# Kernel tuning notes

Measured on AMD Instinct MI355X. Metric: run time of the kernel, lower is better.

## Reference

```python
import jax, jax.numpy as jnp
import numpy as np

B, T = 1024, 512
X_DIM, H_DIM, Z_DIM = 24, 64, 16


def setup_inputs() -> dict:
    key = jax.random.key(0)
    ks = jax.random.split(key, 32)
    w = lambda k, s: jax.random.normal(k, s, jnp.float32) * 0.1
    H, X, Z = H_DIM, X_DIM, Z_DIM
    return {
        "src": jax.random.normal(ks[0], (B, T, X), jnp.float32),
        "eps": jax.random.normal(ks[1], (B, T, Z), jnp.float32),  # reparam noise
        # phi_x: Linear(X,H)+ReLU+Linear(H,H)+ReLU
        "Wx1": w(ks[2], (X, H)), "bx1": w(ks[3], (H,)),
        "Wx2": w(ks[4], (H, H)), "bx2": w(ks[5], (H,)),
        # phi_z: Linear(Z,H)+ReLU
        "Wz": w(ks[6], (Z, H)), "bz": w(ks[7], (H,)),
        # enc: Linear(2H,H)+ReLU+Linear(H,H)+ReLU
        "We1": w(ks[8], (2 * H, H)), "be1": w(ks[9], (H,)),
        "We2": w(ks[10], (H, H)), "be2": w(ks[11], (H,)),
        "Wem": w(ks[12], (H, Z)), "bem": w(ks[13], (Z,)),
        "Wes": w(ks[14], (H, Z)), "bes": w(ks[15], (Z,)),
        # GRU(2H -> H), bias=False; PyTorch gate order r,z,n
        "Wih": w(ks[16], (2 * H, 3 * H)), "Whh": w(ks[17], (H, 3 * H)),
        "Wf1": w(ks[18], (H, H)), "bf1": w(ks[19], (H,)),
        "Wf2": w(ks[20], (H, H // 2)), "bf2": w(ks[21], (H // 2,)),
        "Wf3": w(ks[22], (H // 2, 1)), "bf3": w(ks[23], (1,)),
    }


def _forward(src, eps, Wx1, bx1, Wx2, bx2, Wz, bz, We1, be1, We2, be2,
             Wem, bem, Wes, bes, Wih, Whh, Wf1, bf1, Wf2, bf2, Wf3, bf3):
    relu, sp, sig = jax.nn.relu, jax.nn.softplus, jax.nn.sigmoid
    Bsz = src.shape[0]
    H = Whh.shape[0]

    def step(carry, inp):
        h, _ = carry                      # h: [B, H] (n_layers=1 GRU)
        x_t, e_t = inp                    # [B, X], [B, Z]
        phi_x = relu(relu(x_t @ Wx1 + bx1) @ Wx2 + bx2)
        enc_t = relu(relu(jnp.concatenate([phi_x, h], 1) @ We1 + be1) @ We2 + be2)
        enc_mean = enc_t @ Wem + bem
        enc_std = sp(enc_t @ Wes + bes)
        z_t = e_t * enc_std + enc_mean    # reparameterized sample
        phi_z = relu(z_t @ Wz + bz)
        # GRU cell (bias=False), PyTorch gate order r, z, n
        gi = jnp.concatenate([phi_x, phi_z], 1) @ Wih   # [B, 3H]
        gh = h @ Whh                                    # [B, 3H]
        gir, giz, gin = jnp.split(gi, 3, axis=1)
        ghr, ghz, ghn = jnp.split(gh, 3, axis=1)
        r = sig(gir + ghr)
        u = sig(giz + ghz)
        n = jnp.tanh(gin + r * ghn)
        h_new = (1.0 - u) * n + u * h
        return (h_new, phi_z), None

    h0 = jnp.zeros((Bsz, H), src.dtype)
    xs = jnp.swapaxes(src, 0, 1)   # [T, B, X]
    es = jnp.swapaxes(eps, 0, 1)   # [T, B, Z]
    (_, phi_z), _ = jax.lax.scan(step, (h0, h0), (xs, es))
    out = relu(phi_z @ Wf1 + bf1)
    out = relu(out @ Wf2 + bf2)
    pred = out @ Wf3 + bf3
    return (pred, phi_z)


def reference(src, eps, Wx1, bx1, Wx2, bx2, Wz, bz, We1, be1, We2, be2,
              Wem, bem, Wes, bes, Wih, Whh, Wf1, bf1, Wf2, bf2, Wf3, bf3):
    return _forward(src, eps, Wx1, bx1, Wx2, bx2, Wz, bz, We1, be1, We2, be2,
                    Wem, bem, Wes, bes, Wih, Whh, Wf1, bf1, Wf2, bf2, Wf3, bf3)
```

## Files before the change

kernel.cpp:

```cpp
#include <hip/hip_runtime.h>

#define TT 512
#define BB 1024
#define XD 24
#define ZD 16

typedef __attribute__((ext_vector_type(2))) _Float16 h2t;
typedef __attribute__((ext_vector_type(4))) _Float16 half4;
typedef __attribute__((ext_vector_type(4))) float f32x4;
typedef unsigned long long u64;

__device__ __forceinline__ f32x4 MFMA16(half4 a, half4 b, f32x4 c) {
#if defined(__HIP_DEVICE_COMPILE__)
    return __builtin_amdgcn_mfma_f32_16x16x16f16(a, b, c, 0, 0, 0);
#else
    return c;
#endif
}

__device__ __forceinline__ float rcpf(float x) {
#if defined(__HIP_DEVICE_COMPILE__)
    return __builtin_amdgcn_rcpf(x);
#else
    return 1.0f / x;
#endif
}

__device__ __forceinline__ h2t pkrtz(float a, float b) {
#if defined(__HIP_DEVICE_COMPILE__)
    union { __attribute__((ext_vector_type(2))) __fp16 f; h2t h; } c;
    c.f = __builtin_amdgcn_cvt_pkrtz(a, b);
    return c.h;
#else
    h2t r; r[0] = (_Float16)a; r[1] = (_Float16)b; return r;
#endif
}

#define BAR() asm volatile("s_waitcnt lgkmcnt(0)\n\ts_barrier" ::: "memory")

__device__ __forceinline__ f32x4 Z4() { return (f32x4){0.f, 0.f, 0.f, 0.f}; }

__device__ __forceinline__ float sigm(float x) { return rcpf(1.0f + __expf(-x)); }

__device__ __forceinline__ float tanh_fast(float x) {
    return 1.0f - 2.0f * rcpf(1.0f + __expf(2.0f * x));
}

__device__ __forceinline__ float softplus_f(float x) {
    return fmaxf(x, 0.0f) + __logf(1.0f + __expf(-fabsf(x)));
}

__device__ __forceinline__ half4 ldw(const float* W, int N, int Kreal, int Nreal,
                                     int k0, int o0, int lane) {
    int col = o0 + (lane & 15);
    int kb = k0 + ((lane >> 4) << 2);
    half4 r;
#pragma unroll
    for (int j = 0; j < 4; ++j) {
        int k = kb + j;
        float v = (k < Kreal && col < Nreal) ? W[(size_t)k * N + col] : 0.0f;
        r[j] = (_Float16)v;
    }
    return r;
}

__device__ __forceinline__ half4 cvt_relu(f32x4 a) {
    union { h2t p[2]; half4 h; } c;
    c.p[0] = pkrtz(fmaxf(a[0], 0.f), fmaxf(a[1], 0.f));
    c.p[1] = pkrtz(fmaxf(a[2], 0.f), fmaxf(a[3], 0.f));
    return c.h;
}

__device__ __forceinline__ half4 cvt4(f32x4 a) {
    union { h2t p[2]; half4 h; } c;
    c.p[0] = pkrtz(a[0], a[1]);
    c.p[1] = pkrtz(a[2], a[3]);
    return c.h;
}

__device__ __forceinline__ half4 cvt4_rne(f32x4 a) {
    half4 r;
#pragma unroll
    for (int q = 0; q < 4; ++q) r[q] = (_Float16)a[q];
    return r;
}

__device__ __forceinline__ f32x4 ldb4(const float* b, int o, int lgr) {
    return *reinterpret_cast<const f32x4*>(b + o * 16 + lgr * 4);
}

__device__ __forceinline__ u64 h2u(half4 h) {
    union { half4 h; u64 u; } c; c.h = h; return c.u;
}
__device__ __forceinline__ half4 u2h(u64 u) {
    union { half4 h; u64 u; } c; c.u = u; return c.h;
}

__global__ __launch_bounds__(256, 1) void vrnn_kernel(
    const float* __restrict__ src, const float* __restrict__ eps,
    const float* __restrict__ Wx1, const float* __restrict__ bx1,
    const float* __restrict__ Wx2, const float* __restrict__ bx2,
    const float* __restrict__ Wz,  const float* __restrict__ bz,
    const float* __restrict__ We1, const float* __restrict__ be1,
    const float* __restrict__ We2, const float* __restrict__ be2,
    const float* __restrict__ Wem, const float* __restrict__ bem,
    const float* __restrict__ Wes, const float* __restrict__ bes,
    const float* __restrict__ Wih, const float* __restrict__ Whh,
    const float* __restrict__ Wf1, const float* __restrict__ bf1,
    const float* __restrict__ Wf2, const float* __restrict__ bf2,
    const float* __restrict__ Wf3, const float* __restrict__ bf3,
    float* __restrict__ out)
{
    __shared__ u64 AXB[4 * 64];
    __shared__ u64 A1B[4 * 64];
    __shared__ u64 HB[4 * 64];
    __shared__ u64 PXB[2][4 * 64];

    const int tid = threadIdx.x;
    const int ws = tid >> 6;
    const int lane = tid & 63;
    const int lcol = lane & 15;
    const int lgr = lane >> 4;
    const int r0 = blockIdx.x * 16;
    const int o0w = ws * 16;

    half4 wx1f[2], wx2f[4], we1f[8], we2f[4][4], wemf[4], wesf[4], wzf4[4];
    wx1f[0] = ldw(Wx1, 64, 24, 64, 0, o0w, lane);
    wx1f[1] = ldw(Wx1, 64, 24, 64, 16, o0w, lane);
#pragma unroll
    for (int kt = 0; kt < 4; ++kt) wx2f[kt] = ldw(Wx2, 64, 64, 64, kt * 16, o0w, lane);
#pragma unroll
    for (int kt = 0; kt < 8; ++kt) we1f[kt] = ldw(We1, 64, 128, 64, kt * 16, o0w, lane);
#pragma unroll
    for (int o = 0; o < 4; ++o)
#pragma unroll
        for (int kt = 0; kt < 4; ++kt) we2f[o][kt] = ldw(We2, 64, 64, 64, kt * 16, o * 16, lane);
#pragma unroll
    for (int kt = 0; kt < 4; ++kt) {
        wemf[kt] = ldw(Wem, 16, 64, 16, kt * 16, 0, lane);
        wesf[kt] = ldw(Wes, 16, 64, 16, kt * 16, 0, lane);
    }
#pragma unroll
    for (int o = 0; o < 4; ++o) wzf4[o] = ldw(Wz, 64, 16, 64, 0, o * 16, lane);
    half4 wihf[3][8], whhf[3][4];
#pragma unroll
    for (int g = 0; g < 3; ++g) {
#pragma unroll
        for (int kt = 0; kt < 8; ++kt) wihf[g][kt] = ldw(Wih, 192, 128, 192, kt * 16, g * 64 + o0w, lane);
#pragma unroll
        for (int kt = 0; kt < 4; ++kt) whhf[g][kt] = ldw(Whh, 192, 64, 192, kt * 16, g * 64 + o0w, lane);
    }
    const f32x4 B1 = ldb4(bx1, ws, lgr), B2 = ldb4(bx2, ws, lgr);
    const f32x4 BE1 = ldb4(be1, ws, lgr);
    f32x4 BE2[4], BZf[4];
#pragma unroll
    for (int o = 0; o < 4; ++o) {
        BE2[o] = ldb4(be2, o, lgr);
        BZf[o] = ldb4(bz, o, lgr);
    }
    const f32x4 BM = ldb4(bem, 0, lgr), BS = ldb4(bes, 0, lgr);

    const float* xb_ = src + (size_t)(r0 + lcol) * TT * XD;
    const float* eb_ = eps + (size_t)(r0 + lcol) * TT * ZD;
    float* po = out + BB + (size_t)(r0 + lcol) * 64;

    f32x4 fx0 = *reinterpret_cast<const f32x4*>(xb_ + lgr * 4);
    f32x4 fx1 = Z4();
    if (lgr < 2) fx1 = *reinterpret_cast<const f32x4*>(xb_ + 16 + lgr * 4);
    {
        half4 x0 = cvt4(fx0), x1 = cvt4(fx1);
        f32x4 a = MFMA16(wx1f[1], x1, MFMA16(wx1f[0], x0, B1));
        AXB[ws * 64 + lane] = h2u(cvt_relu(a));
    }
    HB[ws * 64 + lane] = 0ull;
    f32x4 hD = Z4();
    BAR();
    {
        half4 axb[4];
#pragma unroll
        for (int kt = 0; kt < 4; ++kt) axb[kt] = u2h(AXB[kt * 64 + lane]);
        f32x4 a = B2;
#pragma unroll
        for (int kt = 0; kt < 4; ++kt) a = MFMA16(wx2f[kt], axb[kt], a);
        PXB[0][ws * 64 + lane] = h2u(cvt_relu(a));
    }
    fx0 = *reinterpret_cast<const f32x4*>(xb_ + XD + lgr * 4);
    fx1 = Z4();
    if (lgr < 2) fx1 = *reinterpret_cast<const f32x4*>(xb_ + XD + 16 + lgr * 4);
    f32x4 fe = *reinterpret_cast<const f32x4*>(eb_ + lgr * 4);
    BAR();

    half4 pxb[4], pzb[4];

#pragma unroll 1
    for (int t = 0; t < TT; ++t) {
        const size_t t1 = (size_t)((t + 1) & (TT - 1));
        const size_t t2 = (size_t)((t + 2) & (TT - 1));

        half4 hb[4];
#pragma unroll
        for (int kt = 0; kt < 4; ++kt) hb[kt] = u2h(HB[kt * 64 + lane]);
#pragma unroll
        for (int kt = 0; kt < 4; ++kt) pxb[kt] = u2h(PXB[t & 1][kt * 64 + lane]);

        {
            f32x4 a = BE1;
#pragma unroll
            for (int kt = 0; kt < 4; ++kt) a = MFMA16(we1f[kt], pxb[kt], a);
            f32x4 b = Z4();
#pragma unroll
            for (int kt = 0; kt < 4; ++kt) b = MFMA16(we1f[4 + kt], hb[kt], b);
            A1B[ws * 64 + lane] = h2u(cvt_relu(a + b));
        }
        f32x4 ga[3];
#pragma unroll
        for (int g = 0; g < 3; ++g) {
            f32x4 a = MFMA16(whhf[g][1], hb[1], MFMA16(whhf[g][0], hb[0], Z4()));
            f32x4 b = MFMA16(whhf[g][3], hb[3], MFMA16(whhf[g][2], hb[2], Z4()));
            ga[g] = a + b;
        }
        {
            half4 x0 = cvt4(fx0), x1 = cvt4(fx1);
            f32x4 s = MFMA16(wx1f[1], x1, MFMA16(wx1f[0], x0, B1));
            AXB[ws * 64 + lane] = h2u(cvt_relu(s));
            fx0 = *reinterpret_cast<const f32x4*>(xb_ + t2 * XD + lgr * 4);
            fx1 = Z4();
            if (lgr < 2) fx1 = *reinterpret_cast<const f32x4*>(xb_ + t2 * XD + 16 + lgr * 4);
        }
        BAR();

        half4 a1b[4];
#pragma unroll
        for (int kt = 0; kt < 4; ++kt) a1b[kt] = u2h(A1B[kt * 64 + lane]);
        half4 enb[4];
#pragma unroll
        for (int o = 0; o < 4; ++o) {
            f32x4 a = MFMA16(we2f[o][1], a1b[1], MFMA16(we2f[o][0], a1b[0], BE2[o]));
            f32x4 b = MFMA16(we2f[o][3], a1b[3], MFMA16(we2f[o][2], a1b[2], Z4()));
            enb[o] = cvt_relu(a + b);
        }
        f32x4 am = MFMA16(wemf[1], enb[1], MFMA16(wemf[0], enb[0], BM));
        f32x4 am2 = MFMA16(wemf[3], enb[3], MFMA16(wemf[2], enb[2], Z4()));
        f32x4 as_ = MFMA16(wesf[1], enb[1], MFMA16(wesf[0], enb[0], BS));
        f32x4 as2 = MFMA16(wesf[3], enb[3], MFMA16(wesf[2], enb[2], Z4()));
        f32x4 eC = fe;
        fe = *reinterpret_cast<const f32x4*>(eb_ + t1 * ZD + lgr * 4);
        f32x4 zD;
#pragma unroll
        for (int q = 0; q < 4; ++q)
            zD[q] = eC[q] * softplus_f(as_[q] + as2[q]) + (am[q] + am2[q]);
        half4 zb = cvt4(zD);
#pragma unroll
        for (int o = 0; o < 4; ++o) {
            f32x4 a = MFMA16(wzf4[o], zb, BZf[o]);
            if (t == TT - 1 && ws == 0) {
                f32x4 pr;
#pragma unroll
                for (int q = 0; q < 4; ++q) pr[q] = fmaxf(a[q], 0.0f);
                *reinterpret_cast<f32x4*>(po + o * 16 + lgr * 4) = pr;
            }
            pzb[o] = cvt_relu(a);
        }
        f32x4 gi[3];
#pragma unroll
        for (int g = 0; g < 3; ++g) {
            f32x4 p = (g < 2) ? ga[g] : Z4();
#pragma unroll
            for (int kt = 0; kt < 4; ++kt) p = MFMA16(wihf[g][kt], pxb[kt], p);
            f32x4 q = Z4();
#pragma unroll
            for (int kt = 0; kt < 4; ++kt) q = MFMA16(wihf[g][4 + kt], pzb[kt], q);
            gi[g] = p + q;
        }
#pragma unroll
        for (int q = 0; q < 4; ++q) {
            float rr = sigm(gi[0][q]);
            float uu = sigm(gi[1][q]);
            float nn = tanh_fast(gi[2][q] + rr * ga[2][q]);
            hD[q] = (1.0f - uu) * nn + uu * hD[q];
        }
        HB[ws * 64 + lane] = h2u(cvt4_rne(hD));
        {
            half4 axb[4];
#pragma unroll
            for (int kt = 0; kt < 4; ++kt) axb[kt] = u2h(AXB[kt * 64 + lane]);
            f32x4 s = B2;
#pragma unroll
            for (int kt = 0; kt < 4; ++kt) s = MFMA16(wx2f[kt], axb[kt], s);
            PXB[(t + 1) & 1][ws * 64 + lane] = h2u(cvt_relu(s));
        }
        BAR();
    }

    if (ws == 0) {
        half4 wf1t[4][4], wf2t[2][4], wf3t[2];
#pragma unroll
        for (int o = 0; o < 4; ++o)
#pragma unroll
            for (int kt = 0; kt < 4; ++kt) wf1t[o][kt] = ldw(Wf1, 64, 64, 64, kt * 16, o * 16, lane);
#pragma unroll
        for (int o = 0; o < 2; ++o)
#pragma unroll
            for (int kt = 0; kt < 4; ++kt) wf2t[o][kt] = ldw(Wf2, 32, 64, 32, kt * 16, o * 16, lane);
        wf3t[0] = ldw(Wf3, 1, 32, 1, 0, 0, lane);
        wf3t[1] = ldw(Wf3, 1, 32, 1, 16, 0, lane);

        half4 o1b[4];
#pragma unroll
        for (int o = 0; o < 4; ++o) {
            f32x4 a = ldb4(bf1, o, lgr);
#pragma unroll
            for (int kt = 0; kt < 4; ++kt) a = MFMA16(wf1t[o][kt], pzb[kt], a);
            o1b[o] = cvt_relu(a);
        }
        half4 o2b[2];
#pragma unroll
        for (int o = 0; o < 2; ++o) {
            f32x4 a = ldb4(bf2, o, lgr);
#pragma unroll
            for (int kt = 0; kt < 4; ++kt) a = MFMA16(wf2t[o][kt], o1b[kt], a);
            o2b[o] = cvt_relu(a);
        }
        float b3 = bf3[0];
        f32x4 p = (f32x4){b3, b3, b3, b3};
        p = MFMA16(wf3t[0], o2b[0], p);
        p = MFMA16(wf3t[1], o2b[1], p);
        if (lgr == 0) out[r0 + lcol] = p[0];
    }
}

extern "C" void kernel_launch(void* const* d_in, const int* in_sizes, int n_in,
                              void* d_out, int out_size, void* d_ws, size_t ws_size,
                              hipStream_t stream) {
    (void)in_sizes; (void)n_in; (void)d_ws; (void)ws_size; (void)out_size;
    const float* src = (const float*)d_in[0];
    const float* eps = (const float*)d_in[1];
    const float* Wx1 = (const float*)d_in[2];
    const float* bx1 = (const float*)d_in[3];
    const float* Wx2 = (const float*)d_in[4];
    const float* bx2 = (const float*)d_in[5];
    const float* Wz  = (const float*)d_in[6];
    const float* bz  = (const float*)d_in[7];
    const float* We1 = (const float*)d_in[8];
    const float* be1 = (const float*)d_in[9];
    const float* We2 = (const float*)d_in[10];
    const float* be2 = (const float*)d_in[11];
    const float* Wem = (const float*)d_in[12];
    const float* bem = (const float*)d_in[13];
    const float* Wes = (const float*)d_in[14];
    const float* bes = (const float*)d_in[15];
    const float* Wih = (const float*)d_in[16];
    const float* Whh = (const float*)d_in[17];
    const float* Wf1 = (const float*)d_in[18];
    const float* bf1 = (const float*)d_in[19];
    const float* Wf2 = (const float*)d_in[20];
    const float* bf2 = (const float*)d_in[21];
    const float* Wf3 = (const float*)d_in[22];
    const float* bf3 = (const float*)d_in[23];
    float* out = (float*)d_out;

    hipLaunchKernelGGL(vrnn_kernel, dim3(BB / 16), dim3(256), 0, stream,
                       src, eps, Wx1, bx1, Wx2, bx2, Wz, bz, We1, be1, We2, be2,
                       Wem, bem, Wes, bes, Wih, Whh, Wf1, bf1, Wf2, bf2, Wf3, bf3, out);
}
```

Measured before the change: 912.8 us.

## Replicate enc layer-1 per wave and double-buffer buffers to drop a barrier

Each wave now computes the full 64-wide first encoder layer (all four output tiles) in registers instead of one tile shared through LDS. This removes the A1B buffer and the mid-step barrier, leaving one barrier per timestep. The HB and AXB buffers are double-buffered, and the phi_x second layer is software-pipelined one extra step ahead. The cost is four times the We1 MFMA work per wave and more weight registers (32 extra half4), which adds register pressure.

```diff
diff --git a/kernel.cpp b/kernel.cpp
--- a/kernel.cpp
+++ b/kernel.cpp
@@ -111,9 +111,8 @@
     const float* __restrict__ Wf3, const float* __restrict__ bf3,
     float* __restrict__ out)
 {
-    __shared__ u64 AXB[4 * 64];
-    __shared__ u64 A1B[4 * 64];
-    __shared__ u64 HB[4 * 64];
+    __shared__ u64 AXB[2][4 * 64];
+    __shared__ u64 HB[2][4 * 64];
     __shared__ u64 PXB[2][4 * 64];
 
     const int tid = threadIdx.x;
@@ -124,13 +123,15 @@
     const int r0 = blockIdx.x * 16;
     const int o0w = ws * 16;
 
-    half4 wx1f[2], wx2f[4], we1f[8], we2f[4][4], wemf[4], wesf[4], wzf4[4];
+    half4 wx1f[2], wx2f[4], we1f[4][8], we2f[4][4], wemf[4], wesf[4], wzf4[4];
     wx1f[0] = ldw(Wx1, 64, 24, 64, 0, o0w, lane);
     wx1f[1] = ldw(Wx1, 64, 24, 64, 16, o0w, lane);
 #pragma unroll
     for (int kt = 0; kt < 4; ++kt) wx2f[kt] = ldw(Wx2, 64, 64, 64, kt * 16, o0w, lane);
 #pragma unroll
-    for (int kt = 0; kt < 8; ++kt) we1f[kt] = ldw(We1, 64, 128, 64, kt * 16, o0w, lane);
+    for (int o = 0; o < 4; ++o)
+#pragma unroll
+        for (int kt = 0; kt < 8; ++kt) we1f[o][kt] = ldw(We1, 64, 128, 64, kt * 16, o * 16, lane);
 #pragma unroll
     for (int o = 0; o < 4; ++o)
 #pragma unroll
@@ -151,11 +152,11 @@
         for (int kt = 0; kt < 4; ++kt) whhf[g][kt] = ldw(Whh, 192, 64, 192, kt * 16, g * 64 + o0w, lane);
     }
     const f32x4 B1 = ldb4(bx1, ws, lgr), B2 = ldb4(bx2, ws, lgr);
-    const f32x4 BE1 = ldb4(be1, ws, lgr);
-    f32x4 BE2[4], BZf[4];
+    f32x4 BE1f[4], BE2f[4], BZf[4];
 #pragma unroll
     for (int o = 0; o < 4; ++o) {
-        BE2[o] = ldb4(be2, o, lgr);
+        BE1f[o] = ldb4(be1, o, lgr);
+        BE2f[o] = ldb4(be2, o, lgr);
         BZf[o] = ldb4(bz, o, lgr);
     }
     const f32x4 BM = ldb4(bem, 0, lgr), BS = ldb4(bes, 0, lgr);
@@ -170,23 +171,31 @@
     {
         half4 x0 = cvt4(fx0), x1 = cvt4(fx1);
         f32x4 a = MFMA16(wx1f[1], x1, MFMA16(wx1f[0], x0, B1));
-        AXB[ws * 64 + lane] = h2u(cvt_relu(a));
-    }
-    HB[ws * 64 + lane] = 0ull;
+        AXB[1][ws * 64 + lane] = h2u(cvt_relu(a));
+    }
+    HB[0][ws * 64 + lane] = 0ull;
     f32x4 hD = Z4();
+    fx0 = *reinterpret_cast<const f32x4*>(xb_ + XD + lgr * 4);
+    fx1 = Z4();
+    if (lgr < 2) fx1 = *reinterpret_cast<const f32x4*>(xb_ + XD + 16 + lgr * 4);
     BAR();
     {
         half4 axb[4];
 #pragma unroll
-        for (int kt = 0; kt < 4; ++kt) axb[kt] = u2h(AXB[kt * 64 + lane]);
+        for (int kt = 0; kt < 4; ++kt) axb[kt] = u2h(AXB[1][kt * 64 + lane]);
         f32x4 a = B2;
 #pragma unroll
         for (int kt = 0; kt < 4; ++kt) a = MFMA16(wx2f[kt], axb[kt], a);
         PXB[0][ws * 64 + lane] = h2u(cvt_relu(a));
     }
-    fx0 = *reinterpret_cast<const f32x4*>(xb_ + XD + lgr * 4);
+    {
+        half4 x0 = cvt4(fx0), x1 = cvt4(fx1);
+        f32x4 a = MFMA16(wx1f[1], x1, MFMA16(wx1f[0], x0, B1));
+        AXB[0][ws * 64 + lane] = h2u(cvt_relu(a));
+    }
+    fx0 = *reinterpret_cast<const f32x4*>(xb_ + 2 * XD + lgr * 4);
     fx1 = Z4();
-    if (lgr < 2) fx1 = *reinterpret_cast<const f32x4*>(xb_ + XD + 16 + lgr * 4);
+    if (lgr < 2) fx1 = *reinterpret_cast<const f32x4*>(xb_ + 2 * XD + 16 + lgr * 4);
     f32x4 fe = *reinterpret_cast<const f32x4*>(eb_ + lgr * 4);
     BAR();
 
@@ -194,24 +203,18 @@
 
 #pragma unroll 1
     for (int t = 0; t < TT; ++t) {
+        const int cur = t & 1, nxt = (t + 1) & 1;
         const size_t t1 = (size_t)((t + 1) & (TT - 1));
-        const size_t t2 = (size_t)((t + 2) & (TT - 1));
-
-        half4 hb[4];
-#pragma unroll
-        for (int kt = 0; kt < 4; ++kt) hb[kt] = u2h(HB[kt * 64 + lane]);
-#pragma unroll
-        for (int kt = 0; kt < 4; ++kt) pxb[kt] = u2h(PXB[t & 1][kt * 64 + lane]);
-
-        {
-            f32x4 a = BE1;
-#pragma unroll
-            for (int kt = 0; kt < 4; ++kt) a = MFMA16(we1f[kt], pxb[kt], a);
-            f32x4 b = Z4();
-#pragma unroll
-            for (int kt = 0; kt < 4; ++kt) b = MFMA16(we1f[4 + kt], hb[kt], b);
-            A1B[ws * 64 + lane] = h2u(cvt_relu(a + b));
-        }
+        const size_t t3 = (size_t)((t + 3) & (TT - 1));
+
+        half4 hb[4], axb[4];
+#pragma unroll
+        for (int kt = 0; kt < 4; ++kt) hb[kt] = u2h(HB[cur][kt * 64 + lane]);
+#pragma unroll
+        for (int kt = 0; kt < 4; ++kt) pxb[kt] = u2h(PXB[cur][kt * 64 + lane]);
+#pragma unroll
+        for (int kt = 0; kt < 4; ++kt) axb[kt] = u2h(AXB[cur][kt * 64 + lane]);
+
         f32x4 ga[3];
 #pragma unroll
         for (int g = 0; g < 3; ++g) {
@@ -219,23 +222,37 @@
             f32x4 b = MFMA16(whhf[g][3], hb[3], MFMA16(whhf[g][2], hb[2], Z4()));
             ga[g] = a + b;
         }
+
+        half4 a1b[4];
+#pragma unroll
+        for (int o = 0; o < 4; ++o) {
+            f32x4 a = MFMA16(we1f[o][1], pxb[1], MFMA16(we1f[o][0], pxb[0], BE1f[o]));
+            f32x4 b = MFMA16(we1f[o][3], pxb[3], MFMA16(we1f[o][2], pxb[2], Z4()));
+            f32x4 c = MFMA16(we1f[o][5], hb[1], MFMA16(we1f[o][4], hb[0], Z4()));
+            f32x4 d = MFMA16(we1f[o][7], hb[3], MFMA16(we1f[o][6], hb[2], Z4()));
+            a1b[o] = cvt_relu((a + b) + (c + d));
+        }
+
         {
             half4 x0 = cvt4(fx0), x1 = cvt4(fx1);
             f32x4 s = MFMA16(wx1f[1], x1, MFMA16(wx1f[0], x0, B1));
-            AXB[ws * 64 + lane] = h2u(cvt_relu(s));
-            fx0 = *reinterpret_cast<const f32x4*>(xb_ + t2 * XD + lgr * 4);
+            AXB[nxt][ws * 64 + lane] = h2u(cvt_relu(s));
+            fx0 = *reinterpret_cast<const f32x4*>(xb_ + t3 * XD + lgr * 4);
             fx1 = Z4();
-            if (lgr < 2) fx1 = *reinterpret_cast<const f32x4*>(xb_ + t2 * XD + 16 + lgr * 4);
-        }
-        BAR();
-
-        half4 a1b[4];
-#pragma unroll
-        for (int kt = 0; kt < 4; ++kt) a1b[kt] = u2h(A1B[kt * 64 + lane]);
+            if (lgr < 2) fx1 = *reinterpret_cast<const f32x4*>(xb_ + t3 * XD + 16 + lgr * 4);
+        }
+
+        {
+            f32x4 s = B2;
+#pragma unroll
+            for (int kt = 0; kt < 4; ++kt) s = MFMA16(wx2f[kt], axb[kt], s);
+            PXB[nxt][ws * 64 + lane] = h2u(cvt_relu(s));
+        }
+
         half4 enb[4];
 #pragma unroll
         for (int o = 0; o < 4; ++o) {
-            f32x4 a = MFMA16(we2f[o][1], a1b[1], MFMA16(we2f[o][0], a1b[0], BE2[o]));
+            f32x4 a = MFMA16(we2f[o][1], a1b[1], MFMA16(we2f[o][0], a1b[0], BE2f[o]));
             f32x4 b = MFMA16(we2f[o][3], a1b[3], MFMA16(we2f[o][2], a1b[2], Z4()));
             enb[o] = cvt_relu(a + b);
         }
@@ -250,6 +267,7 @@
         for (int q = 0; q < 4; ++q)
             zD[q] = eC[q] * softplus_f(as_[q] + as2[q]) + (am[q] + am2[q]);
         half4 zb = cvt4(zD);
+
 #pragma unroll
         for (int o = 0; o < 4; ++o) {
             f32x4 a = MFMA16(wzf4[o], zb, BZf[o]);
@@ -261,6 +279,7 @@
             }
             pzb[o] = cvt_relu(a);
         }
+
         f32x4 gi[3];
 #pragma unroll
         for (int g = 0; g < 3; ++g) {
@@ -279,16 +298,8 @@
             float nn = tanh_fast(gi[2][q] + rr * ga[2][q]);
             hD[q] = (1.0f - uu) * nn + uu * hD[q];
         }
-        HB[ws * 64 + lane] = h2u(cvt4_rne(hD));
-        {
-            half4 axb[4];
-#pragma unroll
-            for (int kt = 0; kt < 4; ++kt) axb[kt] = u2h(AXB[kt * 64 + lane]);
-            f32x4 s = B2;
-#pragma unroll
-            for (int kt = 0; kt < 4; ++kt) s = MFMA16(wx2f[kt], axb[kt], s);
-            PXB[(t + 1) & 1][ws * 64 + lane] = h2u(cvt_relu(s));
-        }
+        HB[nxt][ws * 64 + lane] = h2u(cvt4_rne(hD));
+
         BAR();
     }
 
```

Result: slower. 1.023 ms (+12.1%).

## Switch recurrent matmuls to 16x16x32 f16 MFMA with paired LDS layout

Applied to the files above, without the earlier changes.

Replaces most 16x16x16 MFMA chains (phi_x, encoder, GRU hidden and input-from-phi_x gates) with the double-K 16x16x32 instruction, halving the MFMA issue count on the serial per-step path. The LDS activation buffers are re-laid out so two adjacent 16-wide K tiles are stored interleaved, letting each lane fetch an 8-half fragment with one 128-bit load. The AXB buffer load is moved earlier, right after the first barrier, and the GRU update is rewritten to use one fewer multiply. The new layout adds indexing complexity and relies on the gfx950 instruction being available.

```diff
diff --git a/kernel.cpp b/kernel.cpp
--- a/kernel.cpp
+++ b/kernel.cpp
@@ -7,12 +7,20 @@
 
 typedef __attribute__((ext_vector_type(2))) _Float16 h2t;
 typedef __attribute__((ext_vector_type(4))) _Float16 half4;
+typedef __attribute__((ext_vector_type(8))) _Float16 half8;
 typedef __attribute__((ext_vector_type(4))) float f32x4;
 typedef unsigned long long u64;
 
 __device__ __forceinline__ f32x4 MFMA16(half4 a, half4 b, f32x4 c) {
 #if defined(__HIP_DEVICE_COMPILE__)
     return __builtin_amdgcn_mfma_f32_16x16x16f16(a, b, c, 0, 0, 0);
+#else
+    return c;
+#endif
+}
+__device__ __forceinline__ f32x4 MFMA32(half8 a, half8 b, f32x4 c) {
+#if defined(__HIP_DEVICE_COMPILE__)
+    return __builtin_amdgcn_mfma_f32_16x16x32_f16(a, b, c, 0, 0, 0);
 #else
     return c;
 #endif
@@ -63,6 +71,19 @@
     }
     return r;
 }
+__device__ __forceinline__ half8 ldw32(const float* W, int N, int Kreal, int Nreal,
+                                       int k0, int o0, int lane) {
+    int col = o0 + (lane & 15);
+    int kb = k0 + ((lane >> 4) << 3);
+    half8 r;
+#pragma unroll
+    for (int j = 0; j < 8; ++j) {
+        int k = kb + j;
+        float v = (k < Kreal && col < Nreal) ? W[(size_t)k * N + col] : 0.0f;
+        r[j] = (_Float16)v;
+    }
+    return r;
+}
 
 __device__ __forceinline__ half4 cvt_relu(f32x4 a) {
     union { h2t p[2]; half4 h; } c;
@@ -70,20 +91,24 @@
     c.p[1] = pkrtz(fmaxf(a[2], 0.f), fmaxf(a[3], 0.f));
     return c.h;
 }
-
 __device__ __forceinline__ half4 cvt4(f32x4 a) {
     union { h2t p[2]; half4 h; } c;
     c.p[0] = pkrtz(a[0], a[1]);
     c.p[1] = pkrtz(a[2], a[3]);
     return c.h;
 }
-
 __device__ __forceinline__ half4 cvt4_rne(f32x4 a) {
     half4 r;
 #pragma unroll
     for (int q = 0; q < 4; ++q) r[q] = (_Float16)a[q];
     return r;
 }
+__device__ __forceinline__ half8 xfrag(f32x4 A, f32x4 B) {
+    union { h2t p[4]; half8 h; } c;
+    c.p[0] = pkrtz(A[0], A[1]); c.p[1] = pkrtz(A[2], A[3]);
+    c.p[2] = pkrtz(B[0], B[1]); c.p[3] = pkrtz(B[2], B[3]);
+    return c.h;
+}
 
 __device__ __forceinline__ f32x4 ldb4(const float* b, int o, int lgr) {
     return *reinterpret_cast<const f32x4*>(b + o * 16 + lgr * 4);
@@ -92,8 +117,12 @@
 __device__ __forceinline__ u64 h2u(half4 h) {
     union { half4 h; u64 u; } c; c.h = h; return c.u;
 }
-__device__ __forceinline__ half4 u2h(u64 u) {
-    union { half4 h; u64 u; } c; c.u = u; return c.h;
+
+__device__ __forceinline__ void st_pair(u64* B, int w, int c, u64 v) {
+    *reinterpret_cast<u64*>(reinterpret_cast<char*>(B) + ((w >> 1) * 256 + c * 16 + (w & 1) * 8)) = v;
+}
+__device__ __forceinline__ half8 ld_pair(const u64* B, int pair, int c) {
+    return *reinterpret_cast<const half8*>(reinterpret_cast<const char*>(B) + pair * 256 + c * 16);
 }
 
 __global__ __launch_bounds__(256, 1) void vrnn_kernel(
@@ -111,10 +140,10 @@
     const float* __restrict__ Wf3, const float* __restrict__ bf3,
     float* __restrict__ out)
 {
-    __shared__ u64 AXB[4 * 64];
-    __shared__ u64 A1B[4 * 64];
-    __shared__ u64 HB[4 * 64];
-    __shared__ u64 PXB[2][4 * 64];
+    __shared__ alignas(16) u64 AXB[256];
+    __shared__ alignas(16) u64 A1B[256];
+    __shared__ alignas(16) u64 HB[256];
+    __shared__ alignas(16) u64 PXB[2][256];
 
     const int tid = threadIdx.x;
     const int ws = tid >> 6;
@@ -123,18 +152,19 @@
     const int lgr = lane >> 4;
     const int r0 = blockIdx.x * 16;
     const int o0w = ws * 16;
-
-    half4 wx1f[2], wx2f[4], we1f[8], we2f[4][4], wemf[4], wesf[4], wzf4[4];
-    wx1f[0] = ldw(Wx1, 64, 24, 64, 0, o0w, lane);
-    wx1f[1] = ldw(Wx1, 64, 24, 64, 16, o0w, lane);
-#pragma unroll
-    for (int kt = 0; kt < 4; ++kt) wx2f[kt] = ldw(Wx2, 64, 64, 64, kt * 16, o0w, lane);
-#pragma unroll
-    for (int kt = 0; kt < 8; ++kt) we1f[kt] = ldw(We1, 64, 128, 64, kt * 16, o0w, lane);
+    const int wsl = ws * 4 + lgr;
+
+    half8 wx1w = ldw32(Wx1, 64, 24, 64, 0, o0w, lane);
+    half8 wx2w[2], we1w[4], we2w[4][2];
+#pragma unroll
+    for (int kt = 0; kt < 2; ++kt) wx2w[kt] = ldw32(Wx2, 64, 64, 64, kt * 32, o0w, lane);
+#pragma unroll
+    for (int kt = 0; kt < 4; ++kt) we1w[kt] = ldw32(We1, 64, 128, 64, kt * 32, o0w, lane);
 #pragma unroll
     for (int o = 0; o < 4; ++o)
 #pragma unroll
-        for (int kt = 0; kt < 4; ++kt) we2f[o][kt] = ldw(We2, 64, 64, 64, kt * 16, o * 16, lane);
+        for (int kt = 0; kt < 2; ++kt) we2w[o][kt] = ldw32(We2, 64, 64, 64, kt * 32, o * 16, lane);
+    half4 wemf[4], wesf[4], wzf4[4];
 #pragma unroll
     for (int kt = 0; kt < 4; ++kt) {
         wemf[kt] = ldw(Wem, 16, 64, 16, kt * 16, 0, lane);
@@ -142,20 +172,25 @@
     }
 #pragma unroll
     for (int o = 0; o < 4; ++o) wzf4[o] = ldw(Wz, 64, 16, 64, 0, o * 16, lane);
-    half4 wihf[3][8], whhf[3][4];
+    half8 wihw[3][2], whhw[3][2];
+    half4 wihz[3][4];
 #pragma unroll
     for (int g = 0; g < 3; ++g) {
 #pragma unroll
-        for (int kt = 0; kt < 8; ++kt) wihf[g][kt] = ldw(Wih, 192, 128, 192, kt * 16, g * 64 + o0w, lane);
-#pragma unroll
-        for (int kt = 0; kt < 4; ++kt) whhf[g][kt] = ldw(Whh, 192, 64, 192, kt * 16, g * 64 + o0w, lane);
+        for (int kt = 0; kt < 2; ++kt) {
+            wihw[g][kt] = ldw32(Wih, 192, 128, 192, kt * 32, g * 64 + o0w, lane);
+            whhw[g][kt] = ldw32(Whh, 192, 64, 192, kt * 32, g * 64 + o0w, lane);
+        }
+#pragma unroll
+        for (int kt = 0; kt < 4; ++kt)
+            wihz[g][kt] = ldw(Wih, 192, 128, 192, 64 + kt * 16, g * 64 + o0w, lane);
     }
     const f32x4 B1 = ldb4(bx1, ws, lgr), B2 = ldb4(bx2, ws, lgr);
     const f32x4 BE1 = ldb4(be1, ws, lgr);
-    f32x4 BE2[4], BZf[4];
+    f32x4 BE2f[4], BZf[4];
 #pragma unroll
     for (int o = 0; o < 4; ++o) {
-        BE2[o] = ldb4(be2, o, lgr);
+        BE2f[o] = ldb4(be2, o, lgr);
         BZf[o] = ldb4(bz, o, lgr);
     }
     const f32x4 BM = ldb4(bem, 0, lgr), BS = ldb4(bes, 0, lgr);
@@ -164,81 +199,76 @@
     const float* eb_ = eps + (size_t)(r0 + lcol) * TT * ZD;
     float* po = out + BB + (size_t)(r0 + lcol) * 64;
 
-    f32x4 fx0 = *reinterpret_cast<const f32x4*>(xb_ + lgr * 4);
-    f32x4 fx1 = Z4();
-    if (lgr < 2) fx1 = *reinterpret_cast<const f32x4*>(xb_ + 16 + lgr * 4);
+    f32x4 fxA = Z4(), fxB = Z4();
+    if (lgr < 3) {
+        fxA = *reinterpret_cast<const f32x4*>(xb_ + lgr * 8);
+        fxB = *reinterpret_cast<const f32x4*>(xb_ + lgr * 8 + 4);
+    }
     {
-        half4 x0 = cvt4(fx0), x1 = cvt4(fx1);
-        f32x4 a = MFMA16(wx1f[1], x1, MFMA16(wx1f[0], x0, B1));
-        AXB[ws * 64 + lane] = h2u(cvt_relu(a));
-    }
-    HB[ws * 64 + lane] = 0ull;
+        f32x4 s = MFMA32(wx1w, xfrag(fxA, fxB), B1);
+        st_pair(A1B, wsl, lcol, h2u(cvt_relu(s)));
+    }
+    HB[tid] = 0ull;
     f32x4 hD = Z4();
+    fxA = Z4(); fxB = Z4();
+    if (lgr < 3) {
+        fxA = *reinterpret_cast<const f32x4*>(xb_ + XD + lgr * 8);
+        fxB = *reinterpret_cast<const f32x4*>(xb_ + XD + lgr * 8 + 4);
+    }
     BAR();
     {
-        half4 axb[4];
-#pragma unroll
-        for (int kt = 0; kt < 4; ++kt) axb[kt] = u2h(AXB[kt * 64 + lane]);
-        f32x4 a = B2;
-#pragma unroll
-        for (int kt = 0; kt < 4; ++kt) a = MFMA16(wx2f[kt], axb[kt], a);
-        PXB[0][ws * 64 + lane] = h2u(cvt_relu(a));
-    }
-    fx0 = *reinterpret_cast<const f32x4*>(xb_ + XD + lgr * 4);
-    fx1 = Z4();
-    if (lgr < 2) fx1 = *reinterpret_cast<const f32x4*>(xb_ + XD + 16 + lgr * 4);
+        half8 a1p0 = ld_pair(A1B, lgr, lcol);
+        half8 a1p1 = ld_pair(A1B, 4 + lgr, lcol);
+        f32x4 s = MFMA32(wx2w[1], a1p1, MFMA32(wx2w[0], a1p0, B2));
+        st_pair(PXB[0], wsl, lcol, h2u(cvt_relu(s)));
+    }
     f32x4 fe = *reinterpret_cast<const f32x4*>(eb_ + lgr * 4);
     BAR();
 
-    half4 pxb[4], pzb[4];
+    half4 pzb[4];
+    half8 pxp0, pxp1;
 
 #pragma unroll 1
     for (int t = 0; t < TT; ++t) {
+        const int cur = t & 1, nxt = cur ^ 1;
         const size_t t1 = (size_t)((t + 1) & (TT - 1));
         const size_t t2 = (size_t)((t + 2) & (TT - 1));
 
-        half4 hb[4];
-#pragma unroll
-        for (int kt = 0; kt < 4; ++kt) hb[kt] = u2h(HB[kt * 64 + lane]);
-#pragma unroll
-        for (int kt = 0; kt < 4; ++kt) pxb[kt] = u2h(PXB[t & 1][kt * 64 + lane]);
+        half8 hp0 = ld_pair(HB, lgr, lcol);
+        half8 hp1 = ld_pair(HB, 4 + lgr, lcol);
+        pxp0 = ld_pair(PXB[cur], lgr, lcol);
+        pxp1 = ld_pair(PXB[cur], 4 + lgr, lcol);
 
         {
-            f32x4 a = BE1;
-#pragma unroll
-            for (int kt = 0; kt < 4; ++kt) a = MFMA16(we1f[kt], pxb[kt], a);
-            f32x4 b = Z4();
-#pragma unroll
-            for (int kt = 0; kt < 4; ++kt) b = MFMA16(we1f[4 + kt], hb[kt], b);
-            A1B[ws * 64 + lane] = h2u(cvt_relu(a + b));
+            f32x4 a = MFMA32(we1w[1], pxp1, MFMA32(we1w[0], pxp0, BE1));
+            f32x4 b = MFMA32(we1w[3], hp1, MFMA32(we1w[2], hp0, Z4()));
+            st_pair(A1B, wsl, lcol, h2u(cvt_relu(a + b)));
         }
         f32x4 ga[3];
 #pragma unroll
-        for (int g = 0; g < 3; ++g) {
-            f32x4 a = MFMA16(whhf[g][1], hb[1], MFMA16(whhf[g][0], hb[0], Z4()));
-            f32x4 b = MFMA16(whhf[g][3], hb[3], MFMA16(whhf[g][2], hb[2], Z4()));
-            ga[g] = a + b;
-        }
+        for (int g = 0; g < 3; ++g)
+            ga[g] = MFMA32(whhw[g][1], hp1, MFMA32(whhw[g][0], hp0, Z4()));
         {
-            half4 x0 = cvt4(fx0), x1 = cvt4(fx1);
-            f32x4 s = MFMA16(wx1f[1], x1, MFMA16(wx1f[0], x0, B1));
-            AXB[ws * 64 + lane] = h2u(cvt_relu(s));
-            fx0 = *reinterpret_cast<const f32x4*>(xb_ + t2 * XD + lgr * 4);
-            fx1 = Z4();
-            if (lgr < 2) fx1 = *reinterpret_cast<const f32x4*>(xb_ + t2 * XD + 16 + lgr * 4);
+            f32x4 s = MFMA32(wx1w, xfrag(fxA, fxB), B1);
+            st_pair(AXB, wsl, lcol, h2u(cvt_relu(s)));
+            fxA = Z4(); fxB = Z4();
+            if (lgr < 3) {
+                fxA = *reinterpret_cast<const f32x4*>(xb_ + t2 * XD + lgr * 8);
+                fxB = *reinterpret_cast<const f32x4*>(xb_ + t2 * XD + lgr * 8 + 4);
+            }
         }
         BAR();
 
-        half4 a1b[4];
-#pragma unroll
-        for (int kt = 0; kt < 4; ++kt) a1b[kt] = u2h(A1B[kt * 64 + lane]);
+        half8 a1p0 = ld_pair(A1B, lgr, lcol);
+        half8 a1p1 = ld_pair(A1B, 4 + lgr, lcol);
+        half8 axp0 = ld_pair(AXB, lgr, lcol);
+        half8 axp1 = ld_pair(AXB, 4 + lgr, lcol);
+
         half4 enb[4];
 #pragma unroll
-        for (int o = 0; o < 4; ++o) {
-            f32x4 a = MFMA16(we2f[o][1], a1b[1], MFMA16(we2f[o][0], a1b[0], BE2[o]));
-            f32x4 b = MFMA16(we2f[o][3], a1b[3], MFMA16(we2f[o][2], a1b[2], Z4()));
-            enb[o] = cvt_relu(a + b);
-        }
+        for (int o = 0; o < 4; ++o)
+            enb[o] = cvt_relu(MFMA32(we2w[o][1], a1p1, MFMA32(we2w[o][0], a1p0, BE2f[o])));
+
         f32x4 am = MFMA16(wemf[1], enb[1], MFMA16(wemf[0], enb[0], BM));
         f32x4 am2 = MFMA16(wemf[3], enb[3], MFMA16(wemf[2], enb[2], Z4()));
         f32x4 as_ = MFMA16(wesf[1], enb[1], MFMA16(wesf[0], enb[0], BS));
@@ -250,6 +280,7 @@
         for (int q = 0; q < 4; ++q)
             zD[q] = eC[q] * softplus_f(as_[q] + as2[q]) + (am[q] + am2[q]);
         half4 zb = cvt4(zD);
+
 #pragma unroll
         for (int o = 0; o < 4; ++o) {
             f32x4 a = MFMA16(wzf4[o], zb, BZf[o]);
@@ -261,33 +292,27 @@
             }
             pzb[o] = cvt_relu(a);
         }
+
         f32x4 gi[3];
 #pragma unroll
         for (int g = 0; g < 3; ++g) {
-            f32x4 p = (g < 2) ? ga[g] : Z4();
-#pragma unroll
-            for (int kt = 0; kt < 4; ++kt) p = MFMA16(wihf[g][kt], pxb[kt], p);
-            f32x4 q = Z4();
-#pragma unroll
-            for (int kt = 0; kt < 4; ++kt) q = MFMA16(wihf[g][4 + kt], pzb[kt], q);
-            gi[g] = p + q;
+            f32x4 p = MFMA32(wihw[g][1], pxp1, MFMA32(wihw[g][0], pxp0, (g < 2) ? ga[g] : Z4()));
+            f32x4 q = MFMA16(wihz[g][1], pzb[1], MFMA16(wihz[g][0], pzb[0], Z4()));
+            f32x4 q2 = MFMA16(wihz[g][3], pzb[3], MFMA16(wihz[g][2], pzb[2], Z4()));
+            gi[g] = p + (q + q2);
         }
 #pragma unroll
         for (int q = 0; q < 4; ++q) {
             float rr = sigm(gi[0][q]);
             float uu = sigm(gi[1][q]);
             float nn = tanh_fast(gi[2][q] + rr * ga[2][q]);
-            hD[q] = (1.0f - uu) * nn + uu * hD[q];
-        }
-        HB[ws * 64 + lane] = h2u(cvt4_rne(hD));
+            hD[q] = nn + uu * (hD[q] - nn);
+        }
+        st_pair(HB, wsl, lcol, h2u(cvt4_rne(hD)));
+
         {
-            half4 axb[4];
-#pragma unroll
-            for (int kt = 0; kt < 4; ++kt) axb[kt] = u2h(AXB[kt * 64 + lane]);
-            f32x4 s = B2;
-#pragma unroll
-            for (int kt = 0; kt < 4; ++kt) s = MFMA16(wx2f[kt], axb[kt], s);
-            PXB[(t + 1) & 1][ws * 64 + lane] = h2u(cvt_relu(s));
+            f32x4 s = MFMA32(wx2w[1], axp1, MFMA32(wx2w[0], axp0, B2));
+            st_pair(PXB[nxt], wsl, lcol, h2u(cvt_relu(s)));
         }
         BAR();
     }
```

After: 786.5 us. 13.8% less time.
